# Kernel optimization log

Measured on AMD Instinct MI355X. Metric: run time of the kernel, lower is better.

Reference implementation:

```python
import jax, jax.numpy as jnp
import numpy as np

LEAKY_ALPHA = 0.2      # nn.LeakyReLU(alpha)
NEG_FILL = -9e15       # zero_vec fill value
BN_EPS = 1e-5          # BatchNorm1d default eps

N, F_IN, F_OUT, E = 8192, 256, 64, 262144


def setup_inputs() -> dict:
    key = jax.random.key(0)
    ks = jax.random.split(key, 4)
    h = jax.random.normal(ks[0], (N, F_IN), jnp.float32)
    edge_index = jax.random.randint(ks[1], (2, E), 0, N, dtype=jnp.int64)
    # xavier_uniform-scale params
    W = jax.random.normal(ks[2], (F_IN, F_OUT), jnp.float32) * (1.0 / np.sqrt(F_IN))
    a = jax.random.normal(ks[3], (2 * F_OUT, 1), jnp.float32) * 0.1
    bias = jnp.zeros((F_OUT,), jnp.float32)   # filled with 0.0 in reset_parameters0
    gamma = jnp.ones((F_OUT,), jnp.float32)   # BatchNorm1d weight
    beta = jnp.zeros((F_OUT,), jnp.float32)   # BatchNorm1d bias
    return {"h": h, "edge_index": edge_index, "W": W, "a": a,
            "bias": bias, "gamma": gamma, "beta": beta}


def reference(h, edge_index, W, a, bias, gamma, beta):
    # --- GATLayer (num_heads=1, concat=True, activation=None, dropout off) ---
    hp = h @ W                                   # [N, F_OUT]
    n = hp.shape[0]
    f = hp.shape[1]
    # a_input @ a with a_input[i,j] = [hp_i ; hp_j] decomposes as f1_i + f2_j
    a1, a2 = a[:f, 0], a[f:, 0]
    f1 = hp @ a1                                 # [N]
    f2 = hp @ a2                                 # [N]
    e = jax.nn.leaky_relu(f1[:, None] + f2[None, :], LEAKY_ALPHA)  # [N, N]
    row, col = edge_index[0], edge_index[1]
    adj = jnp.zeros((n, n), dtype=bool).at[row, col].set(True)
    att = jax.nn.softmax(jnp.where(adj, e, NEG_FILL), axis=1)      # [N, N]
    alpha = att[row, col]                        # [E]
    out = att @ hp                               # [N, F_OUT]
    # BatchNorm1d, training mode: batch stats, biased variance
    mean = jnp.mean(out, axis=0)
    var = jnp.mean((out - mean) ** 2, axis=0)
    out = (out - mean) / jnp.sqrt(var + BN_EPS) * gamma + beta
    out = out + bias                             # activation is None
    return out, alpha
```

## Files before the change

kernel.cpp:

```cpp
#include <hip/hip_runtime.h>
#include <stdint.h>

#define N_NODES 8192
#define F_IN    256
#define F_OUT   64
#define N_EDGES 262144
#define LEAKY   0.2f
#define BN_EPSF 1e-5f
#define WPR     256
#define MAXDEG  256
#define WT_LD   260
#define SLOTS   8

typedef unsigned int u32;

__device__ __forceinline__ float lrelu(float x) {
    return fmaxf(x, LEAKY * x);
}

__global__ __launch_bounds__(256) void k_pre(
    const float* __restrict__ h, const float* __restrict__ W, const float* __restrict__ a,
    float* __restrict__ hp, float* __restrict__ f1, float* __restrict__ f2,
    u32* __restrict__ bm, float* __restrict__ Sacc)
{
    __shared__ float Wt[F_OUT * WT_LD];
    __shared__ float hl[32 * F_IN];
    const int tid = threadIdx.x;

    {
        const float4 z = {0.f, 0.f, 0.f, 0.f};
        float4* dst = reinterpret_cast<float4*>(bm + (size_t)blockIdx.x * 8192);
#pragma unroll
        for (int p = 0; p < 8; ++p) dst[tid + p * 256] = z;
        if (blockIdx.x == 0)
            reinterpret_cast<float4*>(Sacc)[tid] = z;
    }

    const int w = tid >> 6, lane = tid & 63;
#pragma unroll
    for (int t = 0; t < 64; ++t) {
        const int T = t * 4 + w;
        const int o = (T & 7) * 8 + (lane & 7);
        const int k = (T >> 3) * 8 + (lane >> 3);
        Wt[o * WT_LD + k] = W[k * F_OUT + o];
    }

    const int row0 = blockIdx.x * 32;
    float4* hl4 = reinterpret_cast<float4*>(hl);
    const float4* h4 = reinterpret_cast<const float4*>(h + (size_t)row0 * F_IN);
#pragma unroll
    for (int p = 0; p < 8; ++p)
        hl4[tid + p * 256] = h4[tid + p * 256];
    __syncthreads();

    const int rbase = w * 8;
    float acc[8] = {0.f, 0.f, 0.f, 0.f, 0.f, 0.f, 0.f, 0.f};
    const int o = lane;
    for (int q = 0; q < 64; ++q) {
        const float4 wv = *reinterpret_cast<const float4*>(&Wt[o * WT_LD + 4 * q]);
#pragma unroll
        for (int r = 0; r < 8; ++r) {
            const float4 hv = *reinterpret_cast<const float4*>(&hl[(rbase + r) * F_IN + 4 * q]);
            acc[r] += wv.x * hv.x + wv.y * hv.y + wv.z * hv.z + wv.w * hv.w;
        }
    }

    const float a1 = a[o], a2 = a[F_OUT + o];
#pragma unroll
    for (int r = 0; r < 8; ++r) {
        const int row = row0 + rbase + r;
        hp[row * F_OUT + o] = acc[r];
        float p1 = acc[r] * a1;
        float p2 = acc[r] * a2;
#pragma unroll
        for (int off = 32; off; off >>= 1) {
            p1 += __shfl_xor(p1, off, 64);
            p2 += __shfl_xor(p2, off, 64);
        }
        if (o == 0) { f1[row] = p1; f2[row] = p2; }
    }
}

__global__ __launch_bounds__(256) void k_adj(const int* __restrict__ ei, u32* __restrict__ bm)
{
    const int e = blockIdx.x * 256 + threadIdx.x;
    const int r = ei[e];
    const int c = ei[N_EDGES + e];
    atomicOr(&bm[(size_t)r * WPR + (c >> 5)], 1u << (c & 31));
}

__global__ __launch_bounds__(256) void k_attn(
    const u32* __restrict__ bm, const float* __restrict__ hp,
    const float* __restrict__ f1g, const float* __restrict__ f2g,
    float* __restrict__ Mg, float* __restrict__ Dg, float* __restrict__ outr,
    float* __restrict__ Sacc, float* __restrict__ Qacc)
{
    __shared__ int   nbr[4][MAXDEG];
    __shared__ float fv [4][MAXDEG];
    __shared__ int   cnt[4];
    __shared__ float bnS[4][F_OUT], bnQ[4][F_OUT];
    const int tid = threadIdx.x;
    const int w = tid >> 6, lane = tid & 63;
    const int row = blockIdx.x * 4 + w;

    if (lane == 0) cnt[w] = 0;

    float mymax = -1e30f;
    const u32* bmrow = bm + (size_t)row * WPR;
#pragma unroll
    for (int r4 = 0; r4 < 4; ++r4) {
        const int widx = r4 * 64 + lane;
        u32 bits = bmrow[widx];
        if (bits) {
            int pos = atomicAdd(&cnt[w], __popc(bits));
            while (bits) {
                const int b = __ffs(bits) - 1;
                bits &= bits - 1;
                const int j = widx * 32 + b;
                const float v = f2g[j];
                mymax = fmaxf(mymax, v);
                if (pos < MAXDEG) { nbr[w][pos] = j; fv[w][pos] = v; }
                ++pos;
            }
        }
    }
#pragma unroll
    for (int off = 32; off; off >>= 1)
        mymax = fmaxf(mymax, __shfl_xor(mymax, off, 64));

    const int deg = min(cnt[w], MAXDEG);
    const float f1i = f1g[row];
    float M = lrelu(f1i + mymax);

    float den0 = 0.f, den1 = 0.f, acc0 = 0.f, acc1 = 0.f;
    int n = 0;
    for (; n + 2 <= deg; n += 2) {
        const int j0 = nbr[w][n],     j1 = nbr[w][n + 1];
        const float w0 = __expf(lrelu(f1i + fv[w][n]) - M);
        const float w1 = __expf(lrelu(f1i + fv[w][n + 1]) - M);
        den0 += w0;                      den1 += w1;
        acc0 += w0 * hp[j0 * F_OUT + lane];
        acc1 += w1 * hp[j1 * F_OUT + lane];
    }
    if (n < deg) {
        const int j0 = nbr[w][n];
        const float w0 = __expf(lrelu(f1i + fv[w][n]) - M);
        den0 += w0;
        acc0 += w0 * hp[j0 * F_OUT + lane];
    }
    float den = den0 + den1;
    float v = (acc0 + acc1) / den;
    if (deg == 0) { den = 1.f; M = 0.f; v = 0.f; }

    outr[row * F_OUT + lane] = v;
    if (lane == 0) { Mg[row] = M; Dg[row] = den; }

    bnS[w][lane] = v;
    bnQ[w][lane] = v * v;
    __syncthreads();
    if (w == 0) {
        const float s = bnS[0][lane] + bnS[1][lane] + bnS[2][lane] + bnS[3][lane];
        const float q = bnQ[0][lane] + bnQ[1][lane] + bnQ[2][lane] + bnQ[3][lane];
        const int slot = blockIdx.x & (SLOTS - 1);
        atomicAdd(&Sacc[slot * F_OUT + lane], s);
        atomicAdd(&Qacc[slot * F_OUT + lane], q);
    }
}

__global__ __launch_bounds__(256) void k_post(
    const float* __restrict__ outr, const float* __restrict__ Sacc,
    const float* __restrict__ Qacc, const float* __restrict__ gamma,
    const float* __restrict__ beta, const float* __restrict__ bias,
    const int* __restrict__ ei, const float* __restrict__ f1g,
    const float* __restrict__ f2g, const float* __restrict__ Mg,
    const float* __restrict__ Dg, float* __restrict__ out)
{
    const int tid = threadIdx.x;
    if (blockIdx.x < 512) {
        __shared__ float sm[F_OUT], sr[F_OUT], sg[F_OUT], sb[F_OUT];
        if (tid < F_OUT) {
            float s = 0.f, q = 0.f;
#pragma unroll
            for (int k = 0; k < SLOTS; ++k) {
                s += Sacc[k * F_OUT + tid];
                q += Qacc[k * F_OUT + tid];
            }
            const float mean = s * (1.f / N_NODES);
            const float var = q * (1.f / N_NODES) - mean * mean;
            sm[tid] = mean;
            sr[tid] = rsqrtf(var + BN_EPSF);
            sg[tid] = gamma[tid];
            sb[tid] = beta[tid] + bias[tid];
        }
        __syncthreads();
        const int gid = blockIdx.x * 256 + tid;
        const float4 ov = reinterpret_cast<const float4*>(outr)[gid];
        const int o0 = (gid & 15) * 4;
        float4 res;
        res.x = (ov.x - sm[o0 + 0]) * sr[o0 + 0] * sg[o0 + 0] + sb[o0 + 0];
        res.y = (ov.y - sm[o0 + 1]) * sr[o0 + 1] * sg[o0 + 1] + sb[o0 + 1];
        res.z = (ov.z - sm[o0 + 2]) * sr[o0 + 2] * sg[o0 + 2] + sb[o0 + 2];
        res.w = (ov.w - sm[o0 + 3]) * sr[o0 + 3] * sg[o0 + 3] + sb[o0 + 3];
        reinterpret_cast<float4*>(out)[gid] = res;
    } else {
        const int e = (blockIdx.x - 512) * 256 + tid;
        const int r = ei[e];
        const int c = ei[N_EDGES + e];
        out[N_NODES * F_OUT + e] = __expf(lrelu(f1g[r] + f2g[c]) - Mg[r]) / Dg[r];
    }
}

extern "C" void kernel_launch(void* const* d_in, const int* in_sizes, int n_in,
                              void* d_out, int out_size, void* d_ws, size_t ws_size,
                              hipStream_t stream) {
    const float* h     = (const float*)d_in[0];
    const int*   ei    = (const int*)  d_in[1];
    const float* W     = (const float*)d_in[2];
    const float* a     = (const float*)d_in[3];
    const float* bias  = (const float*)d_in[4];
    const float* gamma = (const float*)d_in[5];
    const float* beta  = (const float*)d_in[6];
    float* out = (float*)d_out;

    char* ws = (char*)d_ws;
    float* hp    = (float*)(ws + 0);
    float* f1    = (float*)(ws + 2097152);
    float* f2    = (float*)(ws + 2129920);
    float* Mg    = (float*)(ws + 2162688);
    float* Dg    = (float*)(ws + 2195456);
    float* outr  = (float*)(ws + 2228224);
    float* Sacc  = (float*)(ws + 4325376);
    float* Qacc  = (float*)(ws + 4327424);
    u32*   bm    = (u32*)  (ws + 4329472);
    if (ws_size < (size_t)4329472 + (size_t)N_NODES * WPR * 4) return;

    k_pre <<<256,  256, 0, stream>>>(h, W, a, hp, f1, f2, bm, Sacc);
    k_adj <<<N_EDGES / 256, 256, 0, stream>>>(ei, bm);
    k_attn<<<N_NODES / 4, 256, 0, stream>>>(bm, hp, f1, f2, Mg, Dg, outr, Sacc, Qacc);
    k_post<<<1536, 256, 0, stream>>>(outr, Sacc, Qacc, gamma, beta, bias,
                                     ei, f1, f2, Mg, Dg, out);
}
```

Before: 118.4 us.

## Fuse all four stages into one cooperative kernel with grid syncs

Merges the projection, adjacency build, attention aggregation and BatchNorm/alpha kernels into one cooperative launch of 256 blocks of 1024 threads, separated by grid-wide barriers. This removes three kernel launch gaps. It also stages f2 in shared memory and replaces the shared-memory atomic neighbour counter with a wave prefix scan over uint4 bitmask loads. In exchange, only 256 large blocks run, which lowers occupancy and parallelism in the projection and attention phases, and grid.sync adds barrier cost.

After: 218.7 us. 1.85x slower.

```diff
diff --git a/kernel.cpp b/kernel.cpp
--- a/kernel.cpp
+++ b/kernel.cpp
@@ -1,5 +1,8 @@
 #include <hip/hip_runtime.h>
+#include <hip/hip_cooperative_groups.h>
 #include <stdint.h>
+
+namespace cg = cooperative_groups;
 
 #define N_NODES 8192
 #define F_IN    256
@@ -18,195 +21,203 @@
     return fmaxf(x, LEAKY * x);
 }
 
-__global__ __launch_bounds__(256) void k_pre(
-    const float* __restrict__ h, const float* __restrict__ W, const float* __restrict__ a,
+struct P1 {
+    float Wt[F_OUT * WT_LD];
+    float hl[32 * F_IN];
+};
+struct P3 {
+    float f2l[N_NODES];
+    float bnS[16][F_OUT];
+    float bnQ[16][F_OUT];
+    int   nbr[16][MAXDEG];
+    float fv [16][MAXDEG];
+};
+
+__global__ __launch_bounds__(1024, 4) void k_all(
+    const float* __restrict__ h, const int* __restrict__ ei,
+    const float* __restrict__ W, const float* __restrict__ a,
+    const float* __restrict__ bias, const float* __restrict__ gamma,
+    const float* __restrict__ beta,
     float* __restrict__ hp, float* __restrict__ f1, float* __restrict__ f2,
-    u32* __restrict__ bm, float* __restrict__ Sacc)
+    float* __restrict__ Mg, float* __restrict__ Dg, float* __restrict__ outr,
+    float* __restrict__ Sacc, float* __restrict__ Qacc,
+    u32* __restrict__ bm, float* __restrict__ out)
 {
-    __shared__ float Wt[F_OUT * WT_LD];
-    __shared__ float hl[32 * F_IN];
+    __shared__ union { P1 p1; P3 p3; } S;
+    cg::grid_group grid = cg::this_grid();
     const int tid = threadIdx.x;
+    const int w = tid >> 6, lane = tid & 63;
+    const int b = blockIdx.x;
+    const int row0 = b * 32;
 
     {
         const float4 z = {0.f, 0.f, 0.f, 0.f};
-        float4* dst = reinterpret_cast<float4*>(bm + (size_t)blockIdx.x * 8192);
-#pragma unroll
-        for (int p = 0; p < 8; ++p) dst[tid + p * 256] = z;
-        if (blockIdx.x == 0)
+        float4* dst = reinterpret_cast<float4*>(bm + (size_t)b * (32 * WPR));
+        dst[tid] = z; dst[tid + 1024] = z;
+        if (b == 0 && tid < 256)
             reinterpret_cast<float4*>(Sacc)[tid] = z;
     }
-
-    const int w = tid >> 6, lane = tid & 63;
-#pragma unroll
-    for (int t = 0; t < 64; ++t) {
-        const int T = t * 4 + w;
+#pragma unroll
+    for (int t = 0; t < 16; ++t) {
+        const int T = t * 16 + w;
         const int o = (T & 7) * 8 + (lane & 7);
         const int k = (T >> 3) * 8 + (lane >> 3);
-        Wt[o * WT_LD + k] = W[k * F_OUT + o];
-    }
-
-    const int row0 = blockIdx.x * 32;
-    float4* hl4 = reinterpret_cast<float4*>(hl);
-    const float4* h4 = reinterpret_cast<const float4*>(h + (size_t)row0 * F_IN);
-#pragma unroll
-    for (int p = 0; p < 8; ++p)
-        hl4[tid + p * 256] = h4[tid + p * 256];
-    __syncthreads();
-
-    const int rbase = w * 8;
-    float acc[8] = {0.f, 0.f, 0.f, 0.f, 0.f, 0.f, 0.f, 0.f};
-    const int o = lane;
-    for (int q = 0; q < 64; ++q) {
-        const float4 wv = *reinterpret_cast<const float4*>(&Wt[o * WT_LD + 4 * q]);
-#pragma unroll
-        for (int r = 0; r < 8; ++r) {
-            const float4 hv = *reinterpret_cast<const float4*>(&hl[(rbase + r) * F_IN + 4 * q]);
-            acc[r] += wv.x * hv.x + wv.y * hv.y + wv.z * hv.z + wv.w * hv.w;
-        }
-    }
-
-    const float a1 = a[o], a2 = a[F_OUT + o];
-#pragma unroll
-    for (int r = 0; r < 8; ++r) {
-        const int row = row0 + rbase + r;
-        hp[row * F_OUT + o] = acc[r];
-        float p1 = acc[r] * a1;
-        float p2 = acc[r] * a2;
+        S.p1.Wt[o * WT_LD + k] = W[k * F_OUT + o];
+    }
+    {
+        float4* hl4 = reinterpret_cast<float4*>(S.p1.hl);
+        const float4* h4 = reinterpret_cast<const float4*>(h + (size_t)row0 * F_IN);
+        hl4[tid] = h4[tid]; hl4[tid + 1024] = h4[tid + 1024];
+    }
+    __syncthreads();
+    {
+        const int o = lane;
+        const float* hr0 = &S.p1.hl[(w * 2 + 0) * F_IN];
+        const float* hr1 = &S.p1.hl[(w * 2 + 1) * F_IN];
+        float acc0 = 0.f, acc1 = 0.f;
+        for (int q = 0; q < 64; ++q) {
+            const float4 wv = *reinterpret_cast<const float4*>(&S.p1.Wt[o * WT_LD + 4 * q]);
+            const float4 h0 = *reinterpret_cast<const float4*>(&hr0[4 * q]);
+            const float4 h1 = *reinterpret_cast<const float4*>(&hr1[4 * q]);
+            acc0 += wv.x * h0.x + wv.y * h0.y + wv.z * h0.z + wv.w * h0.w;
+            acc1 += wv.x * h1.x + wv.y * h1.y + wv.z * h1.z + wv.w * h1.w;
+        }
+        const int row = row0 + w * 2;
+        hp[row * F_OUT + o] = acc0;
+        hp[(row + 1) * F_OUT + o] = acc1;
+        const float a1v = a[o], a2v = a[F_OUT + o];
+        float p10 = acc0 * a1v, p20 = acc0 * a2v;
+        float p11 = acc1 * a1v, p21 = acc1 * a2v;
 #pragma unroll
         for (int off = 32; off; off >>= 1) {
-            p1 += __shfl_xor(p1, off, 64);
-            p2 += __shfl_xor(p2, off, 64);
-        }
-        if (o == 0) { f1[row] = p1; f2[row] = p2; }
-    }
-}
-
-__global__ __launch_bounds__(256) void k_adj(const int* __restrict__ ei, u32* __restrict__ bm)
-{
-    const int e = blockIdx.x * 256 + threadIdx.x;
-    const int r = ei[e];
-    const int c = ei[N_EDGES + e];
-    atomicOr(&bm[(size_t)r * WPR + (c >> 5)], 1u << (c & 31));
-}
-
-__global__ __launch_bounds__(256) void k_attn(
-    const u32* __restrict__ bm, const float* __restrict__ hp,
-    const float* __restrict__ f1g, const float* __restrict__ f2g,
-    float* __restrict__ Mg, float* __restrict__ Dg, float* __restrict__ outr,
-    float* __restrict__ Sacc, float* __restrict__ Qacc)
-{
-    __shared__ int   nbr[4][MAXDEG];
-    __shared__ float fv [4][MAXDEG];
-    __shared__ int   cnt[4];
-    __shared__ float bnS[4][F_OUT], bnQ[4][F_OUT];
-    const int tid = threadIdx.x;
-    const int w = tid >> 6, lane = tid & 63;
-    const int row = blockIdx.x * 4 + w;
-
-    if (lane == 0) cnt[w] = 0;
-
-    float mymax = -1e30f;
-    const u32* bmrow = bm + (size_t)row * WPR;
-#pragma unroll
-    for (int r4 = 0; r4 < 4; ++r4) {
-        const int widx = r4 * 64 + lane;
-        u32 bits = bmrow[widx];
-        if (bits) {
-            int pos = atomicAdd(&cnt[w], __popc(bits));
+            p10 += __shfl_xor(p10, off, 64);
+            p20 += __shfl_xor(p20, off, 64);
+            p11 += __shfl_xor(p11, off, 64);
+            p21 += __shfl_xor(p21, off, 64);
+        }
+        if (o == 0) {
+            f1[row] = p10; f2[row] = p20;
+            f1[row + 1] = p11; f2[row + 1] = p21;
+        }
+    }
+    grid.sync();
+
+    {
+        const int e = b * 1024 + tid;
+        const int r = ei[e];
+        const int c = ei[N_EDGES + e];
+        atomicOr(&bm[(size_t)r * WPR + (c >> 5)], 1u << (c & 31));
+    }
+    grid.sync();
+
+    {
+        float4* f2l4 = reinterpret_cast<float4*>(S.p3.f2l);
+        const float4* f24 = reinterpret_cast<const float4*>(f2);
+        f2l4[tid] = f24[tid]; f2l4[tid + 1024] = f24[tid + 1024];
+    }
+    __syncthreads();
+
+    float myS = 0.f, myQ = 0.f;
+    int* nb = S.p3.nbr[w];
+    float* fvv = S.p3.fv[w];
+    for (int rr = 0; rr < 2; ++rr) {
+        const int row = row0 + w * 2 + rr;
+        const uint4 bw = reinterpret_cast<const uint4*>(bm + (size_t)row * WPR)[lane];
+        const int tot = __popc(bw.x) + __popc(bw.y) + __popc(bw.z) + __popc(bw.w);
+        int pref = tot;
+#pragma unroll
+        for (int off = 1; off < 64; off <<= 1) {
+            const int t2 = __shfl_up(pref, off, 64);
+            if (lane >= off) pref += t2;
+        }
+        const int deg = __shfl(pref, 63, 64);
+        int pos = pref - tot;
+        float mymax = -1e30f;
+        const u32 words[4] = {bw.x, bw.y, bw.z, bw.w};
+#pragma unroll
+        for (int i = 0; i < 4; ++i) {
+            u32 bits = words[i];
+            const int jbase = (lane * 4 + i) * 32;
             while (bits) {
-                const int b = __ffs(bits) - 1;
+                const int bit = __ffs(bits) - 1;
                 bits &= bits - 1;
-                const int j = widx * 32 + b;
-                const float v = f2g[j];
+                const int j = jbase + bit;
+                const float v = S.p3.f2l[j];
                 mymax = fmaxf(mymax, v);
-                if (pos < MAXDEG) { nbr[w][pos] = j; fv[w][pos] = v; }
+                if (pos < MAXDEG) { nb[pos] = j; fvv[pos] = v; }
                 ++pos;
             }
         }
-    }
-#pragma unroll
-    for (int off = 32; off; off >>= 1)
-        mymax = fmaxf(mymax, __shfl_xor(mymax, off, 64));
-
-    const int deg = min(cnt[w], MAXDEG);
-    const float f1i = f1g[row];
-    float M = lrelu(f1i + mymax);
-
-    float den0 = 0.f, den1 = 0.f, acc0 = 0.f, acc1 = 0.f;
-    int n = 0;
-    for (; n + 2 <= deg; n += 2) {
-        const int j0 = nbr[w][n],     j1 = nbr[w][n + 1];
-        const float w0 = __expf(lrelu(f1i + fv[w][n]) - M);
-        const float w1 = __expf(lrelu(f1i + fv[w][n + 1]) - M);
-        den0 += w0;                      den1 += w1;
-        acc0 += w0 * hp[j0 * F_OUT + lane];
-        acc1 += w1 * hp[j1 * F_OUT + lane];
-    }
-    if (n < deg) {
-        const int j0 = nbr[w][n];
-        const float w0 = __expf(lrelu(f1i + fv[w][n]) - M);
-        den0 += w0;
-        acc0 += w0 * hp[j0 * F_OUT + lane];
-    }
-    float den = den0 + den1;
-    float v = (acc0 + acc1) / den;
-    if (deg == 0) { den = 1.f; M = 0.f; v = 0.f; }
-
-    outr[row * F_OUT + lane] = v;
-    if (lane == 0) { Mg[row] = M; Dg[row] = den; }
-
-    bnS[w][lane] = v;
-    bnQ[w][lane] = v * v;
-    __syncthreads();
-    if (w == 0) {
-        const float s = bnS[0][lane] + bnS[1][lane] + bnS[2][lane] + bnS[3][lane];
-        const float q = bnQ[0][lane] + bnQ[1][lane] + bnQ[2][lane] + bnQ[3][lane];
-        const int slot = blockIdx.x & (SLOTS - 1);
-        atomicAdd(&Sacc[slot * F_OUT + lane], s);
-        atomicAdd(&Qacc[slot * F_OUT + lane], q);
-    }
-}
-
-__global__ __launch_bounds__(256) void k_post(
-    const float* __restrict__ outr, const float* __restrict__ Sacc,
-    const float* __restrict__ Qacc, const float* __restrict__ gamma,
-    const float* __restrict__ beta, const float* __restrict__ bias,
-    const int* __restrict__ ei, const float* __restrict__ f1g,
-    const float* __restrict__ f2g, const float* __restrict__ Mg,
-    const float* __restrict__ Dg, float* __restrict__ out)
-{
-    const int tid = threadIdx.x;
-    if (blockIdx.x < 512) {
-        __shared__ float sm[F_OUT], sr[F_OUT], sg[F_OUT], sb[F_OUT];
-        if (tid < F_OUT) {
-            float s = 0.f, q = 0.f;
-#pragma unroll
-            for (int k = 0; k < SLOTS; ++k) {
-                s += Sacc[k * F_OUT + tid];
-                q += Qacc[k * F_OUT + tid];
-            }
-            const float mean = s * (1.f / N_NODES);
-            const float var = q * (1.f / N_NODES) - mean * mean;
-            sm[tid] = mean;
-            sr[tid] = rsqrtf(var + BN_EPSF);
-            sg[tid] = gamma[tid];
-            sb[tid] = beta[tid] + bias[tid];
-        }
-        __syncthreads();
-        const int gid = blockIdx.x * 256 + tid;
+#pragma unroll
+        for (int off = 32; off; off >>= 1)
+            mymax = fmaxf(mymax, __shfl_xor(mymax, off, 64));
+
+        const int dg = min(deg, MAXDEG);
+        const float f1i = f1[row];
+        float M = lrelu(f1i + mymax);
+        float den0 = 0.f, den1 = 0.f, ac0 = 0.f, ac1 = 0.f;
+        int n = 0;
+        for (; n + 2 <= dg; n += 2) {
+            const int j0 = nb[n], j1 = nb[n + 1];
+            const float w0 = __expf(lrelu(f1i + fvv[n]) - M);
+            const float w1 = __expf(lrelu(f1i + fvv[n + 1]) - M);
+            den0 += w0;  den1 += w1;
+            ac0 += w0 * hp[j0 * F_OUT + lane];
+            ac1 += w1 * hp[j1 * F_OUT + lane];
+        }
+        if (n < dg) {
+            const float w0 = __expf(lrelu(f1i + fvv[n]) - M);
+            den0 += w0;
+            ac0 += w0 * hp[nb[n] * F_OUT + lane];
+        }
+        float den = den0 + den1;
+        float v = (ac0 + ac1) / den;
+        if (dg == 0) { den = 1.f; M = 0.f; v = 0.f; }
+        outr[row * F_OUT + lane] = v;
+        if (lane == 0) { Mg[row] = M; Dg[row] = den; }
+        myS += v; myQ += v * v;
+    }
+    S.p3.bnS[w][lane] = myS;
+    S.p3.bnQ[w][lane] = myQ;
+    __syncthreads();
+    if (tid < F_OUT) {
+        float s = 0.f, q = 0.f;
+#pragma unroll
+        for (int k = 0; k < 16; ++k) { s += S.p3.bnS[k][tid]; q += S.p3.bnQ[k][tid]; }
+        const int slot = b & (SLOTS - 1);
+        atomicAdd(&Sacc[slot * F_OUT + tid], s);
+        atomicAdd(&Qacc[slot * F_OUT + tid], q);
+    }
+    grid.sync();
+
+    if (tid < F_OUT) {
+        float s = 0.f, q = 0.f;
+#pragma unroll
+        for (int k = 0; k < SLOTS; ++k) { s += Sacc[k * F_OUT + tid]; q += Qacc[k * F_OUT + tid]; }
+        const float mean = s * (1.f / N_NODES);
+        const float var = q * (1.f / N_NODES) - mean * mean;
+        S.p3.bnS[0][tid] = mean;
+        S.p3.bnS[1][tid] = rsqrtf(var + BN_EPSF);
+        S.p3.bnS[2][tid] = gamma[tid];
+        S.p3.bnS[3][tid] = beta[tid] + bias[tid];
+    }
+    __syncthreads();
+    if (tid < 512) {
+        const int gid = b * 512 + tid;
         const float4 ov = reinterpret_cast<const float4*>(outr)[gid];
         const int o0 = (gid & 15) * 4;
         float4 res;
-        res.x = (ov.x - sm[o0 + 0]) * sr[o0 + 0] * sg[o0 + 0] + sb[o0 + 0];
-        res.y = (ov.y - sm[o0 + 1]) * sr[o0 + 1] * sg[o0 + 1] + sb[o0 + 1];
-        res.z = (ov.z - sm[o0 + 2]) * sr[o0 + 2] * sg[o0 + 2] + sb[o0 + 2];
-        res.w = (ov.w - sm[o0 + 3]) * sr[o0 + 3] * sg[o0 + 3] + sb[o0 + 3];
+        res.x = (ov.x - S.p3.bnS[0][o0 + 0]) * S.p3.bnS[1][o0 + 0] * S.p3.bnS[2][o0 + 0] + S.p3.bnS[3][o0 + 0];
+        res.y = (ov.y - S.p3.bnS[0][o0 + 1]) * S.p3.bnS[1][o0 + 1] * S.p3.bnS[2][o0 + 1] + S.p3.bnS[3][o0 + 1];
+        res.z = (ov.z - S.p3.bnS[0][o0 + 2]) * S.p3.bnS[1][o0 + 2] * S.p3.bnS[2][o0 + 2] + S.p3.bnS[3][o0 + 2];
+        res.w = (ov.w - S.p3.bnS[0][o0 + 3]) * S.p3.bnS[1][o0 + 3] * S.p3.bnS[2][o0 + 3] + S.p3.bnS[3][o0 + 3];
         reinterpret_cast<float4*>(out)[gid] = res;
-    } else {
-        const int e = (blockIdx.x - 512) * 256 + tid;
+    }
+    {
+        const int e = b * 1024 + tid;
         const int r = ei[e];
         const int c = ei[N_EDGES + e];
-        out[N_NODES * F_OUT + e] = __expf(lrelu(f1g[r] + f2g[c]) - Mg[r]) / Dg[r];
+        out[N_NODES * F_OUT + e] = __expf(lrelu(f1[r] + S.p3.f2l[c]) - Mg[r]) / Dg[r];
     }
 }
 
@@ -234,9 +245,9 @@
     u32*   bm    = (u32*)  (ws + 4329472);
     if (ws_size < (size_t)4329472 + (size_t)N_NODES * WPR * 4) return;
 
-    k_pre <<<256,  256, 0, stream>>>(h, W, a, hp, f1, f2, bm, Sacc);
-    k_adj <<<N_EDGES / 256, 256, 0, stream>>>(ei, bm);
-    k_attn<<<N_NODES / 4, 256, 0, stream>>>(bm, hp, f1, f2, Mg, Dg, outr, Sacc, Qacc);
-    k_post<<<1536, 256, 0, stream>>>(outr, Sacc, Qacc, gamma, beta, bias,
-                                     ei, f1, f2, Mg, Dg, out);
+    void* args[] = {(void*)&h, (void*)&ei, (void*)&W, (void*)&a, (void*)&bias,
+                    (void*)&gamma, (void*)&beta, (void*)&hp, (void*)&f1, (void*)&f2,
+                    (void*)&Mg, (void*)&Dg, (void*)&outr, (void*)&Sacc, (void*)&Qacc,
+                    (void*)&bm, (void*)&out};
+    hipLaunchCooperativeKernel((void*)k_all, dim3(256), dim3(1024), args, 0, stream);
 }
```

## Read h directly from global in projection, wave-scan neighbor compaction, unroll aggregation

Applied to the files above, without the earlier changes.

The projection kernel drops the shared-memory staging of h and reads each row's float4s straight from global memory with a wave-uniform base pointer, cutting LDS usage and the staging barrier at the cost of more global/cache traffic. The attention kernel loads each row's bitmask as one uint4 per lane and computes neighbor positions with a wave prefix-sum instead of shared-memory atomics. The neighbor compaction is also ordered by column. The weighted aggregation loop is unrolled to four independent accumulators to expose more memory-level parallelism.

Measured after the change: 122.2 us. 1.03x slower.

```diff
diff --git a/kernel.cpp b/kernel.cpp
--- a/kernel.cpp
+++ b/kernel.cpp
@@ -24,19 +24,19 @@
     u32* __restrict__ bm, float* __restrict__ Sacc)
 {
     __shared__ float Wt[F_OUT * WT_LD];
-    __shared__ float hl[32 * F_IN];
     const int tid = threadIdx.x;
+    const int w = tid >> 6, lane = tid & 63;
+    const int b = blockIdx.x;
 
     {
         const float4 z = {0.f, 0.f, 0.f, 0.f};
-        float4* dst = reinterpret_cast<float4*>(bm + (size_t)blockIdx.x * 8192);
+        float4* dst = reinterpret_cast<float4*>(bm + (size_t)b * 8192);
 #pragma unroll
         for (int p = 0; p < 8; ++p) dst[tid + p * 256] = z;
-        if (blockIdx.x == 0)
+        if (b == 0 && tid < 256)
             reinterpret_cast<float4*>(Sacc)[tid] = z;
     }
 
-    const int w = tid >> 6, lane = tid & 63;
 #pragma unroll
     for (int t = 0; t < 64; ++t) {
         const int T = t * 4 + w;
@@ -44,31 +44,27 @@
         const int k = (T >> 3) * 8 + (lane >> 3);
         Wt[o * WT_LD + k] = W[k * F_OUT + o];
     }
-
-    const int row0 = blockIdx.x * 32;
-    float4* hl4 = reinterpret_cast<float4*>(hl);
-    const float4* h4 = reinterpret_cast<const float4*>(h + (size_t)row0 * F_IN);
-#pragma unroll
-    for (int p = 0; p < 8; ++p)
-        hl4[tid + p * 256] = h4[tid + p * 256];
     __syncthreads();
 
-    const int rbase = w * 8;
+    const int row0 = b * 32;
+    const int wu = __builtin_amdgcn_readfirstlane(w);
+    const float* hb = h + (size_t)(row0 + wu * 8) * F_IN;
+    const int o = lane;
+
     float acc[8] = {0.f, 0.f, 0.f, 0.f, 0.f, 0.f, 0.f, 0.f};
-    const int o = lane;
     for (int q = 0; q < 64; ++q) {
         const float4 wv = *reinterpret_cast<const float4*>(&Wt[o * WT_LD + 4 * q]);
 #pragma unroll
         for (int r = 0; r < 8; ++r) {
-            const float4 hv = *reinterpret_cast<const float4*>(&hl[(rbase + r) * F_IN + 4 * q]);
-            acc[r] += wv.x * hv.x + wv.y * hv.y + wv.z * hv.z + wv.w * hv.w;
+            const float4 hq = *reinterpret_cast<const float4*>(&hb[r * F_IN + 4 * q]);
+            acc[r] += wv.x * hq.x + wv.y * hq.y + wv.z * hq.z + wv.w * hq.w;
         }
     }
 
     const float a1 = a[o], a2 = a[F_OUT + o];
 #pragma unroll
     for (int r = 0; r < 8; ++r) {
-        const int row = row0 + rbase + r;
+        const int row = row0 + wu * 8 + r;
         hp[row * F_OUT + o] = acc[r];
         float p1 = acc[r] * a1;
         float p2 = acc[r] * a2;
@@ -97,60 +93,70 @@
 {
     __shared__ int   nbr[4][MAXDEG];
     __shared__ float fv [4][MAXDEG];
-    __shared__ int   cnt[4];
     __shared__ float bnS[4][F_OUT], bnQ[4][F_OUT];
     const int tid = threadIdx.x;
     const int w = tid >> 6, lane = tid & 63;
     const int row = blockIdx.x * 4 + w;
 
-    if (lane == 0) cnt[w] = 0;
-
+    const uint4 bw = reinterpret_cast<const uint4*>(bm + (size_t)row * WPR)[lane];
+    const int tot = __popc(bw.x) + __popc(bw.y) + __popc(bw.z) + __popc(bw.w);
+    int pref = tot;
+#pragma unroll
+    for (int off = 1; off < 64; off <<= 1) {
+        const int t2 = __shfl_up(pref, off, 64);
+        if (lane >= off) pref += t2;
+    }
+    const int deg0 = __shfl(pref, 63, 64);
+    int pos = pref - tot;
     float mymax = -1e30f;
-    const u32* bmrow = bm + (size_t)row * WPR;
-#pragma unroll
-    for (int r4 = 0; r4 < 4; ++r4) {
-        const int widx = r4 * 64 + lane;
-        u32 bits = bmrow[widx];
-        if (bits) {
-            int pos = atomicAdd(&cnt[w], __popc(bits));
-            while (bits) {
-                const int b = __ffs(bits) - 1;
-                bits &= bits - 1;
-                const int j = widx * 32 + b;
-                const float v = f2g[j];
-                mymax = fmaxf(mymax, v);
-                if (pos < MAXDEG) { nbr[w][pos] = j; fv[w][pos] = v; }
-                ++pos;
-            }
+    const u32 words[4] = {bw.x, bw.y, bw.z, bw.w};
+    int* nb = nbr[w];
+    float* fvv = fv[w];
+#pragma unroll
+    for (int i = 0; i < 4; ++i) {
+        u32 bits = words[i];
+        const int jbase = (lane * 4 + i) * 32;
+        while (bits) {
+            const int bit = __ffs(bits) - 1;
+            bits &= bits - 1;
+            const int j = jbase + bit;
+            const float v = f2g[j];
+            mymax = fmaxf(mymax, v);
+            if (pos < MAXDEG) { nb[pos] = j; fvv[pos] = v; }
+            ++pos;
         }
     }
 #pragma unroll
     for (int off = 32; off; off >>= 1)
         mymax = fmaxf(mymax, __shfl_xor(mymax, off, 64));
 
-    const int deg = min(cnt[w], MAXDEG);
+    const int dg = min(deg0, MAXDEG);
     const float f1i = f1g[row];
     float M = lrelu(f1i + mymax);
 
-    float den0 = 0.f, den1 = 0.f, acc0 = 0.f, acc1 = 0.f;
+    float den0 = 0.f, den1 = 0.f, den2 = 0.f, den3 = 0.f;
+    float ac0 = 0.f, ac1 = 0.f, ac2 = 0.f, ac3 = 0.f;
     int n = 0;
-    for (; n + 2 <= deg; n += 2) {
-        const int j0 = nbr[w][n],     j1 = nbr[w][n + 1];
-        const float w0 = __expf(lrelu(f1i + fv[w][n]) - M);
-        const float w1 = __expf(lrelu(f1i + fv[w][n + 1]) - M);
-        den0 += w0;                      den1 += w1;
-        acc0 += w0 * hp[j0 * F_OUT + lane];
-        acc1 += w1 * hp[j1 * F_OUT + lane];
-    }
-    if (n < deg) {
-        const int j0 = nbr[w][n];
-        const float w0 = __expf(lrelu(f1i + fv[w][n]) - M);
+    for (; n + 4 <= dg; n += 4) {
+        const int j0 = nb[n], j1 = nb[n + 1], j2 = nb[n + 2], j3 = nb[n + 3];
+        const float w0 = __expf(lrelu(f1i + fvv[n]) - M);
+        const float w1 = __expf(lrelu(f1i + fvv[n + 1]) - M);
+        const float w2 = __expf(lrelu(f1i + fvv[n + 2]) - M);
+        const float w3 = __expf(lrelu(f1i + fvv[n + 3]) - M);
+        den0 += w0; den1 += w1; den2 += w2; den3 += w3;
+        ac0 += w0 * hp[j0 * F_OUT + lane];
+        ac1 += w1 * hp[j1 * F_OUT + lane];
+        ac2 += w2 * hp[j2 * F_OUT + lane];
+        ac3 += w3 * hp[j3 * F_OUT + lane];
+    }
+    for (; n < dg; ++n) {
+        const float w0 = __expf(lrelu(f1i + fvv[n]) - M);
         den0 += w0;
-        acc0 += w0 * hp[j0 * F_OUT + lane];
-    }
-    float den = den0 + den1;
-    float v = (acc0 + acc1) / den;
-    if (deg == 0) { den = 1.f; M = 0.f; v = 0.f; }
+        ac0 += w0 * hp[nb[n] * F_OUT + lane];
+    }
+    float den = (den0 + den1) + (den2 + den3);
+    float v = ((ac0 + ac1) + (ac2 + ac3)) / den;
+    if (dg == 0) { den = 1.f; M = 0.f; v = 0.f; }
 
     outr[row * F_OUT + lane] = v;
     if (lane == 0) { Mg[row] = M; Dg[row] = den; }
```
